# Kernel tuning notes

Measured on AMD Instinct MI355X. Metric: run time of the kernel, lower is better.

The kernel has to match this reference:

```python
import jax, jax.numpy as jnp
import numpy as np

T, B, IN = 64, 4096, 145
H1, H2 = 150, 32


def _lstm_layer(x, w_ih, w_hh, b_ih, b_hh):
    """Single LSTM layer, PyTorch gate order (i, f, g, o).
    x: (T, B, in_dim); w_ih: (4H, in_dim); w_hh: (4H, H); biases: (4H,).
    Returns hidden sequence (T, B, H)."""
    H = w_hh.shape[1]
    Bsz = x.shape[1]
    # Precompute input contribution for all timesteps at once (one big GEMM).
    xg = jnp.einsum('tbi,gi->tbg', x, w_ih) + (b_ih + b_hh)  # (T, B, 4H)
    w_hh_t = w_hh.T  # (H, 4H)

    def step(carry, xg_t):
        h, c = carry
        gates = xg_t + h @ w_hh_t  # (B, 4H)
        i, f, g, o = jnp.split(gates, 4, axis=-1)
        i = jax.nn.sigmoid(i)
        f = jax.nn.sigmoid(f)
        g = jnp.tanh(g)
        o = jax.nn.sigmoid(o)
        c = f * c + i * g
        h = o * jnp.tanh(c)
        return (h, c), h

    h0 = jnp.zeros((Bsz, H), x.dtype)
    c0 = jnp.zeros((Bsz, H), x.dtype)
    _, hs = jax.lax.scan(step, (h0, c0), xg)
    return hs  # (T, B, H)


def _init_lstm_params(key, in_dim, hidden):
    # PyTorch init: U(-k, k) with k = 1/sqrt(hidden)
    k = 1.0 / np.sqrt(hidden)
    ks = jax.random.split(key, 4)
    w_ih = jax.random.uniform(ks[0], (4 * hidden, in_dim), jnp.float32, -k, k)
    w_hh = jax.random.uniform(ks[1], (4 * hidden, hidden), jnp.float32, -k, k)
    b_ih = jax.random.uniform(ks[2], (4 * hidden,), jnp.float32, -k, k)
    b_hh = jax.random.uniform(ks[3], (4 * hidden,), jnp.float32, -k, k)
    return w_ih, w_hh, b_ih, b_hh


def setup_inputs() -> dict:
    key = jax.random.key(0)
    kx, k0, k1, k2 = jax.random.split(key, 4)
    x = jax.random.normal(kx, (T, B, IN), jnp.float32)
    w_ih_l0, w_hh_l0, b_ih_l0, b_hh_l0 = _init_lstm_params(k0, IN, H1)
    w_ih_l1, w_hh_l1, b_ih_l1, b_hh_l1 = _init_lstm_params(k1, H1, H1)
    w_ih_l2, w_hh_l2, b_ih_l2, b_hh_l2 = _init_lstm_params(k2, H1, H2)
    return {
        'x': x,
        'w_ih_l0': w_ih_l0, 'w_hh_l0': w_hh_l0, 'b_ih_l0': b_ih_l0, 'b_hh_l0': b_hh_l0,
        'w_ih_l1': w_ih_l1, 'w_hh_l1': w_hh_l1, 'b_ih_l1': b_ih_l1, 'b_hh_l1': b_hh_l1,
        'w_ih_l2': w_ih_l2, 'w_hh_l2': w_hh_l2, 'b_ih_l2': b_ih_l2, 'b_hh_l2': b_hh_l2,
    }


def reference(x,
              w_ih_l0, w_hh_l0, b_ih_l0, b_hh_l0,
              w_ih_l1, w_hh_l1, b_ih_l1, b_hh_l1,
              w_ih_l2, w_hh_l2, b_ih_l2, b_hh_l2):
    # temporal_model1: 2-layer LSTM (145 -> 150 -> 150)
    h = _lstm_layer(x, w_ih_l0, w_hh_l0, b_ih_l0, b_hh_l0)
    h = _lstm_layer(h, w_ih_l1, w_hh_l1, b_ih_l1, b_hh_l1)
    # temporal_model2: 1-layer LSTM (150 -> 32)
    out2 = _lstm_layer(h, w_ih_l2, w_hh_l2, b_ih_l2, b_hh_l2)
    return out2  # (T, B, 32)
```

## Files before the change

### kernel.cpp

```cpp
#include <hip/hip_runtime.h>


typedef _Float16 f16;
typedef _Float16 f16x8 __attribute__((ext_vector_type(8)));
typedef _Float16 f16x4 __attribute__((ext_vector_type(4)));
typedef float f32x4 __attribute__((ext_vector_type(4)));

#define T_STEPS 64
#define BATCH 4096

__device__ __forceinline__ float fexp(float x) {
  return __builtin_amdgcn_exp2f(x * 1.44269504088896340736f);
}
__device__ __forceinline__ float sigf(float x) {
  return __builtin_amdgcn_rcpf(1.0f + fexp(-x));
}
__device__ __forceinline__ float tanh_f(float x) {
  return 1.0f - 2.0f * __builtin_amdgcn_rcpf(1.0f + fexp(2.0f * x));
}

#define BAR_LGKM() asm volatile("s_waitcnt lgkmcnt(0)\n\ts_barrier" ::: "memory")

__global__ __launch_bounds__(256) void prep_w(
    const float* __restrict__ wih0, const float* __restrict__ bih0, const float* __restrict__ bhh0,
    const float* __restrict__ wih1, const float* __restrict__ bih1, const float* __restrict__ bhh1,
    f16* __restrict__ wprep0, f16* __restrict__ wprep1,
    float* __restrict__ bias0, float* __restrict__ bias1) {
  int idx = blockIdx.x * 256 + threadIdx.x;
  constexpr int WE = 640 * 168;
  if (idx < WE) {
    int c = idx / 168, k = idx - c * 168;
    int gate = c / 160, cg = c - gate * 160;
    float v = (cg < 150 && k < 145) ? wih0[(size_t)(gate * 150 + cg) * 145 + k] : 0.f;
    wprep0[idx] = (f16)v;
  } else if (idx < 2 * WE) {
    int e = idx - WE;
    int c = e / 168, k = e - c * 168;
    int gate = c / 160, cg = c - gate * 160;
    float v = (cg < 150 && k < 150) ? wih1[(size_t)(gate * 150 + cg) * 150 + k] : 0.f;
    wprep1[e] = (f16)v;
  } else if (idx < 2 * WE + 640) {
    int c = idx - 2 * WE;
    int gate = c / 160, cg = c - gate * 160;
    bias0[c] = (cg < 150) ? (bih0[gate * 150 + cg] + bhh0[gate * 150 + cg]) : 0.f;
  } else if (idx < 2 * WE + 1280) {
    int c = idx - 2 * WE - 640;
    int gate = c / 160, cg = c - gate * 160;
    bias1[c] = (cg < 150) ? (bih1[gate * 150 + cg] + bhh1[gate * 150 + cg]) : 0.f;
  }
}

template <int IN_DIM, int SRC_F16>
__global__ __launch_bounds__(512, 4) void gemm_xg4(
    const float* __restrict__ xin_f32, const f16* __restrict__ xin_f16,
    const f16* __restrict__ wprep, const float* __restrict__ bias_pre,
    f16* __restrict__ xg) {
  constexpr int ASTR = 168;
  __shared__ __align__(16) f16 A_lds[128 * ASTR];
  __shared__ __align__(16) f16 W_lds[64 * ASTR];
  __shared__ __align__(16) float bias_lds[640];
  const int tid = threadIdx.x;
  const int mtile = blockIdx.x;
  const int g0 = mtile * 128;

  if constexpr (SRC_F16) {
#pragma unroll
    for (int q = 0; q < 6; ++q) {
      int i = q * 512 + tid;
      if (i < 2688)
        *(f16x8*)(&A_lds[i * 8]) = *(const f16x8*)(xin_f16 + (size_t)g0 * ASTR + (size_t)i * 8);
    }
  } else {
#pragma unroll
    for (int q = 0; q < 10; ++q) {
      int idx = q * 512 + tid;
      int r = idx / 40, c4 = (idx - r * 40) * 4;
      f16x4 o;
      if (c4 + 4 <= IN_DIM) {
        f32x4 v;
        __builtin_memcpy(&v, xin_f32 + (size_t)(g0 + r) * IN_DIM + c4, 16);
#pragma unroll
        for (int j = 0; j < 4; ++j) o[j] = (f16)v[j];
      } else {
#pragma unroll
        for (int j = 0; j < 4; ++j)
          o[j] = (c4 + j < IN_DIM) ? (f16)xin_f32[(size_t)(g0 + r) * IN_DIM + c4 + j] : (f16)0.f;
      }
      *(f16x4*)(&A_lds[r * ASTR + c4]) = o;
    }
  }
  if (tid < 160) *(f32x4*)(&bias_lds[tid * 4]) = *(const f32x4*)(bias_pre + tid * 4);
#pragma unroll
  for (int q = 0; q < 3; ++q) {
    int i = q * 512 + tid;
    if (i < 1344) *(f16x8*)(&W_lds[i * 8]) = *(const f16x8*)(wprep + (size_t)i * 8);
  }
  BAR_LGKM();

  const int l = tid & 63, wv = tid >> 6;
  const int p = wv >> 1, cq = wv & 1;
  const int lrow = l & 15, lk8 = (l >> 4) * 8, r0 = (l >> 4) * 4;
  const int arow0 = (2 * p) * 16 + lrow;
  const int wrow0 = (2 * cq) * 16 + lrow;

  f16x8 pv0, pv1, pv2;
  for (int ch = 0; ch < 10; ++ch) {
    if (ch < 9) {
      const f16* wsrc = wprep + (size_t)(ch + 1) * 10752;
      pv0 = *(const f16x8*)(wsrc + (size_t)tid * 8);
      pv1 = *(const f16x8*)(wsrc + (size_t)(tid + 512) * 8);
      if (tid < 320) pv2 = *(const f16x8*)(wsrc + (size_t)(tid + 1024) * 8);
    }
    const int c0 = ch * 64 + (2 * cq) * 16 + lrow;
    const float bs0 = bias_lds[c0], bs1 = bias_lds[c0 + 16];
    f32x4 a00 = {bs0, bs0, bs0, bs0}, a01 = {bs1, bs1, bs1, bs1};
    f32x4 a10 = a00, a11 = a01;
#pragma unroll
    for (int kc = 0; kc < 5; ++kc) {
      f16x8 a0 = *(const f16x8*)(&A_lds[arow0 * ASTR + kc * 32 + lk8]);
      f16x8 a1 = *(const f16x8*)(&A_lds[(arow0 + 16) * ASTR + kc * 32 + lk8]);
      f16x8 b0 = *(const f16x8*)(&W_lds[wrow0 * ASTR + kc * 32 + lk8]);
      f16x8 b1 = *(const f16x8*)(&W_lds[(wrow0 + 16) * ASTR + kc * 32 + lk8]);
      a00 = __builtin_amdgcn_mfma_f32_16x16x32_f16(a0, b0, a00, 0, 0, 0);
      a01 = __builtin_amdgcn_mfma_f32_16x16x32_f16(a0, b1, a01, 0, 0, 0);
      a10 = __builtin_amdgcn_mfma_f32_16x16x32_f16(a1, b0, a10, 0, 0, 0);
      a11 = __builtin_amdgcn_mfma_f32_16x16x32_f16(a1, b1, a11, 0, 0, 0);
    }
    {
      f16x4 o;
      size_t rg0 = (size_t)(mtile * 8 + 2 * p);
#pragma unroll
      for (int j = 0; j < 4; ++j) o[j] = (f16)a00[j];
      *(f16x4*)(xg + (rg0 * 640 + c0) * 16 + r0) = o;
#pragma unroll
      for (int j = 0; j < 4; ++j) o[j] = (f16)a01[j];
      *(f16x4*)(xg + (rg0 * 640 + c0 + 16) * 16 + r0) = o;
#pragma unroll
      for (int j = 0; j < 4; ++j) o[j] = (f16)a10[j];
      *(f16x4*)(xg + ((rg0 + 1) * 640 + c0) * 16 + r0) = o;
#pragma unroll
      for (int j = 0; j < 4; ++j) o[j] = (f16)a11[j];
      *(f16x4*)(xg + ((rg0 + 1) * 640 + c0 + 16) * 16 + r0) = o;
    }
    if (ch < 9) {
      BAR_LGKM();
      *(f16x8*)(&W_lds[tid * 8]) = pv0;
      *(f16x8*)(&W_lds[(tid + 512) * 8]) = pv1;
      if (tid < 320) *(f16x8*)(&W_lds[(tid + 1024) * 8]) = pv2;
      BAR_LGKM();
    }
  }
}

__global__ __launch_bounds__(640, 2) void lstm_rec(
    const f16* __restrict__ xg, const float* __restrict__ whh,
    f16* __restrict__ hout) {
  constexpr int H = 150, HSTR = 168, CPAD = 640;
  __shared__ __align__(16) f16 hbuf[2][16 * HSTR];
  const int tid = threadIdx.x;
  const int l = tid & 63, w = tid >> 6;
  const int lrow = l & 15, lk8 = (l >> 4) * 8, r0 = (l >> 4) * 4;
  const int col = w * 16 + lrow;
  const int bx = blockIdx.x, b0 = bx * 16;

  for (int i = tid; i < 2 * 16 * HSTR / 8; i += 640) {
    f16x8 z = {};
    *(f16x8*)(&hbuf[0][0] + (size_t)i * 8) = z;
  }

  f16x8 wh[4][5];
#pragma unroll
  for (int g = 0; g < 4; ++g)
#pragma unroll
    for (int kc = 0; kc < 5; ++kc) {
      f16x8 v;
#pragma unroll
      for (int j = 0; j < 8; ++j) {
        int k = kc * 32 + lk8 + j;
        float x = (col < H && k < H) ? whh[((size_t)g * H + col) * H + k] : 0.f;
        v[j] = (f16)x;
      }
      wh[g][kc] = v;
    }
  __syncthreads();

  float creg[4] = {0.f, 0.f, 0.f, 0.f};
  f16x4 pv[4];
#pragma unroll
  for (int g = 0; g < 4; ++g)
    pv[g] = *(const f16x4*)(xg + ((size_t)bx * CPAD + g * 160 + col) * 16 + r0);

  for (int t = 0; t < T_STEPS; ++t) {
    const int cur = t & 1, nxt = cur ^ 1;

    f32x4 acc[4];
#pragma unroll
    for (int g = 0; g < 4; ++g) {
#pragma unroll
      for (int j = 0; j < 4; ++j) acc[g][j] = (float)pv[g][j];
    }
    if (t + 1 < T_STEPS) {
#pragma unroll
      for (int g = 0; g < 4; ++g)
        pv[g] = *(const f16x4*)(xg + ((size_t)((t + 1) * 256 + bx) * CPAD + g * 160 + col) * 16 + r0);
    }
    if (t > 0 && tid < 336) {
      f16x8 v = *(const f16x8*)(&hbuf[cur][tid * 8]);
      *(f16x8*)(hout + ((size_t)(t - 1) * BATCH + b0) * 168 + (size_t)tid * 8) = v;
    }

#pragma unroll
    for (int kc = 0; kc < 5; ++kc) {
      f16x8 a = *(const f16x8*)(&hbuf[cur][lrow * HSTR + kc * 32 + lk8]);
#pragma unroll
      for (int g = 0; g < 4; ++g)
        acc[g] = __builtin_amdgcn_mfma_f32_16x16x32_f16(a, wh[g][kc], acc[g], 0, 0, 0);
    }

#pragma unroll
    for (int j = 0; j < 4; ++j) {
      float iv = sigf(acc[0][j]);
      float fv = sigf(acc[1][j]);
      float gv = tanh_f(acc[2][j]);
      float ov = sigf(acc[3][j]);
      float c = fv * creg[j] + iv * gv;
      creg[j] = c;
      float h = ov * tanh_f(c);
      hbuf[nxt][(r0 + j) * HSTR + col] = (f16)h;
    }

    BAR_LGKM();
  }
  if (tid < 336) {
    f16x8 v = *(const f16x8*)(&hbuf[0][tid * 8]);
    *(f16x8*)(hout + ((size_t)(T_STEPS - 1) * BATCH + b0) * 168 + (size_t)tid * 8) = v;
  }
}

template <int IN_DIM, int H, int MODE>
__global__ __launch_bounds__(512, 2) void lstm_layer(
    const float* __restrict__ xin_f32, const f16* __restrict__ xin_f16,
    const float* __restrict__ w_ih, const float* __restrict__ w_hh,
    const float* __restrict__ b_ih, const float* __restrict__ b_hh,
    f16* __restrict__ hout, float* __restrict__ yout) {
  constexpr int KX = (IN_DIM + 31) / 32;
  constexpr int XSTR = KX * 32 + 8;
  constexpr int KH = (H + 31) / 32;
  constexpr int HSTR = KH * 32 + 8;
  constexpr int NPAD = ((H + 31) / 32) * 32;
  constexpr int NT = NPAD / 32;
  constexpr int GROUPS = NPAD * 4;
  constexpr int UPD_ITERS = (GROUPS + 511) / 512;
  constexpr int XIN_ELEMS = 16 * IN_DIM;
  constexpr int QX = (XIN_ELEMS + 511) / 512;
  constexpr int STG = (16 * XSTR) / 8;
  constexpr int HCP = (16 * HSTR) / 8;
  static_assert(MODE == 0 || XSTR == 168, "");

  __shared__ __align__(16) f16 xbuf[2][16 * XSTR];
  __shared__ __align__(16) f16 hbuf[16 * HSTR];
  __shared__ __align__(16) float gates[NPAD * 84];

  const int tid = threadIdx.x;
  const int l = tid & 63;
  const int wv = tid >> 6;
  const int gate = wv >> 1;
  const int half = wv & 1;
  const int lrow = l & 15;
  const int lk8 = (l >> 4) * 8;
  const int r0 = (l >> 4) * 4;
  const int b0 = blockIdx.x * 16;

  {
    f16* xf = &xbuf[0][0];
    for (int i = tid; i < 2 * 16 * XSTR; i += 512) xf[i] = (f16)0.f;
    for (int i = tid; i < 16 * HSTR; i += 512) hbuf[i] = (f16)0.f;
  }
  const int rbase = half * (NPAD / 2) + lrow;
  float bias_reg[NT];
#pragma unroll
  for (int nt = 0; nt < NT; ++nt) {
    int n = rbase + nt * 16;
    bias_reg[nt] = (n < H) ? (b_ih[gate * H + n] + b_hh[gate * H + n]) : 0.f;
  }
  f16x8 wx[KX][NT], wh[KH][NT];
#pragma unroll
  for (int kc = 0; kc < KX; ++kc)
#pragma unroll
    for (int nt = 0; nt < NT; ++nt) {
      f16x8 wq;
#pragma unroll
      for (int j = 0; j < 8; ++j) {
        int k = kc * 32 + lk8 + j;
        int r = rbase + nt * 16;
        float v = (r < H && k < IN_DIM) ? w_ih[(size_t)(gate * H + r) * IN_DIM + k] : 0.f;
        wq[j] = (f16)v;
      }
      wx[kc][nt] = wq;
    }
#pragma unroll
  for (int kc = 0; kc < KH; ++kc)
#pragma unroll
    for (int nt = 0; nt < NT; ++nt) {
      f16x8 wq;
#pragma unroll
      for (int j = 0; j < 8; ++j) {
        int k = kc * 32 + lk8 + j;
        int r = rbase + nt * 16;
        float v = (r < H && k < H) ? w_hh[(size_t)(gate * H + r) * H + k] : 0.f;
        wq[j] = (f16)v;
      }
      wh[kc][nt] = wq;
    }

  if constexpr (MODE == 0) {
#pragma unroll
    for (int q = 0; q < QX; ++q) {
      int idx = q * 512 + tid;
      if (idx < XIN_ELEMS) {
        float v = xin_f32[(size_t)b0 * IN_DIM + idx];
        int r = idx / IN_DIM, c = idx - r * IN_DIM;
        xbuf[0][r * XSTR + c] = (f16)v;
      }
    }
  } else {
    if (tid < STG) {
      f16x8 v = *(const f16x8*)(xin_f16 + (size_t)b0 * 168 + tid * 8);
      *(f16x8*)(&xbuf[0][tid * 8]) = v;
    }
  }
  __syncthreads();

  float creg[UPD_ITERS][4];
#pragma unroll
  for (int it = 0; it < UPD_ITERS; ++it)
#pragma unroll
    for (int j = 0; j < 4; ++j) creg[it][j] = 0.f;

  float xv[QX];
  f16x8 pv;

  for (int t = 0; t < T_STEPS; ++t) {
    const int cur = t & 1, nxt = cur ^ 1;
    if (t + 1 < T_STEPS) {
      if constexpr (MODE == 0) {
        const float* src = xin_f32 + ((size_t)(t + 1) * BATCH + b0) * IN_DIM;
#pragma unroll
        for (int q = 0; q < QX; ++q) {
          int idx = q * 512 + tid;
          xv[q] = (idx < XIN_ELEMS) ? src[idx] : 0.f;
        }
      } else {
        if (tid < STG)
          pv = *(const f16x8*)(xin_f16 + ((size_t)(t + 1) * BATCH + b0) * 168 + tid * 8);
      }
    }
    if constexpr (MODE != 2) {
      if (t > 0 && tid < HCP) {
        f16x8 v = *(const f16x8*)(&hbuf[tid * 8]);
        *(f16x8*)(hout + ((size_t)(t - 1) * BATCH + b0) * 168 + tid * 8) = v;
      }
    }
    f32x4 acc[NT];
#pragma unroll
    for (int nt = 0; nt < NT; ++nt) {
      float b = bias_reg[nt];
      acc[nt] = f32x4{b, b, b, b};
    }
    {
      const f16* xb = &xbuf[cur][0];
#pragma unroll
      for (int kc = 0; kc < KX; ++kc) {
        f16x8 a = *(const f16x8*)(xb + lrow * XSTR + kc * 32 + lk8);
#pragma unroll
        for (int nt = 0; nt < NT; ++nt)
          acc[nt] = __builtin_amdgcn_mfma_f32_16x16x32_f16(a, wx[kc][nt], acc[nt], 0, 0, 0);
      }
#pragma unroll
      for (int kc = 0; kc < KH; ++kc) {
        f16x8 a = *(const f16x8*)(hbuf + lrow * HSTR + kc * 32 + lk8);
#pragma unroll
        for (int nt = 0; nt < NT; ++nt)
          acc[nt] = __builtin_amdgcn_mfma_f32_16x16x32_f16(a, wh[kc][nt], acc[nt], 0, 0, 0);
      }
    }
#pragma unroll
    for (int nt = 0; nt < NT; ++nt) {
      int n = half * (NPAD / 2) + nt * 16 + lrow;
      *(f32x4*)(&gates[n * 84 + gate * 20 + r0]) = acc[nt];
    }
    BAR_LGKM();
    if (t + 1 < T_STEPS) {
      if constexpr (MODE == 0) {
#pragma unroll
        for (int q = 0; q < QX; ++q) {
          int idx = q * 512 + tid;
          if (idx < XIN_ELEMS) {
            int r = idx / IN_DIM, c = idx - r * IN_DIM;
            xbuf[nxt][r * XSTR + c] = (f16)xv[q];
          }
        }
      } else {
        if (tid < STG) *(f16x8*)(&xbuf[nxt][tid * 8]) = pv;
      }
    }
#pragma unroll
    for (int it = 0; it < UPD_ITERS; ++it) {
      int grp = it * 512 + tid;
      if (grp < GROUPS) {
        int n = grp % NPAD;
        int rb = (grp / NPAD) * 4;
        if (n < H) {
          f32x4 gi = *(const f32x4*)(&gates[n * 84 + 0 + rb]);
          f32x4 gf = *(const f32x4*)(&gates[n * 84 + 20 + rb]);
          f32x4 gg = *(const f32x4*)(&gates[n * 84 + 40 + rb]);
          f32x4 go = *(const f32x4*)(&gates[n * 84 + 60 + rb]);
#pragma unroll
          for (int j = 0; j < 4; ++j) {
            float iv = sigf(gi[j]);
            float fv = sigf(gf[j]);
            float gv = tanh_f(gg[j]);
            float ov = sigf(go[j]);
            float c = fv * creg[it][j] + iv * gv;
            creg[it][j] = c;
            float h = ov * tanh_f(c);
            hbuf[(rb + j) * HSTR + n] = (f16)h;
            if constexpr (MODE == 2) {
              yout[((size_t)t * BATCH + b0 + rb + j) * 32 + n] = h;
            }
          }
        }
      }
    }
    BAR_LGKM();
  }
  if constexpr (MODE != 2) {
    if (tid < HCP) {
      f16x8 v = *(const f16x8*)(&hbuf[tid * 8]);
      *(f16x8*)(hout + ((size_t)(T_STEPS - 1) * BATCH + b0) * 168 + tid * 8) = v;
    }
  }
}

extern "C" void kernel_launch(void* const* d_in, const int* in_sizes, int n_in,
                              void* d_out, int out_size, void* d_ws, size_t ws_size,
                              hipStream_t stream) {
  const float* x = (const float*)d_in[0];
  const float* wih0 = (const float*)d_in[1];
  const float* whh0 = (const float*)d_in[2];
  const float* bih0 = (const float*)d_in[3];
  const float* bhh0 = (const float*)d_in[4];
  const float* wih1 = (const float*)d_in[5];
  const float* whh1 = (const float*)d_in[6];
  const float* bih1 = (const float*)d_in[7];
  const float* bhh1 = (const float*)d_in[8];
  const float* wih2 = (const float*)d_in[9];
  const float* whh2 = (const float*)d_in[10];
  const float* bih2 = (const float*)d_in[11];
  const float* bhh2 = (const float*)d_in[12];

  const size_t HSEQ_BYTES = (size_t)T_STEPS * BATCH * 168 * sizeof(f16);
  const size_t XG_BYTES = (size_t)T_STEPS * BATCH * 640 * sizeof(f16);
  const size_t WPREP_BYTES = (size_t)640 * 168 * sizeof(f16);
  const size_t NEED = HSEQ_BYTES + XG_BYTES + 2 * WPREP_BYTES + 2 * 640 * sizeof(float);
  f16* hws = (f16*)d_ws;
  float* out = (float*)d_out;

  if (ws_size >= NEED) {
    char* base = (char*)d_ws;
    f16* xgbuf = (f16*)(base + HSEQ_BYTES);
    f16* wprep0 = (f16*)(base + HSEQ_BYTES + XG_BYTES);
    f16* wprep1 = (f16*)(base + HSEQ_BYTES + XG_BYTES + WPREP_BYTES);
    float* bias0 = (float*)(base + HSEQ_BYTES + XG_BYTES + 2 * WPREP_BYTES);
    float* bias1 = bias0 + 640;

    prep_w<<<dim3(846), dim3(256), 0, stream>>>(wih0, bih0, bhh0, wih1, bih1, bhh1,
                                                wprep0, wprep1, bias0, bias1);
    dim3 gg(2048), gb(512);
    dim3 rg(BATCH / 16), rb(640);
    gemm_xg4<145, 0><<<gg, gb, 0, stream>>>(x, nullptr, wprep0, bias0, xgbuf);
    lstm_rec<<<rg, rb, 0, stream>>>(xgbuf, whh0, hws);
    gemm_xg4<150, 1><<<gg, gb, 0, stream>>>(nullptr, hws, wprep1, bias1, xgbuf);
    lstm_rec<<<rg, rb, 0, stream>>>(xgbuf, whh1, hws);
    lstm_layer<150, 32, 2><<<dim3(BATCH / 16), dim3(512), 0, stream>>>(
        nullptr, hws, wih2, whh2, bih2, bhh2, nullptr, out);
  } else {
    dim3 grid(BATCH / 16), block(512);
    lstm_layer<145, 150, 0><<<grid, block, 0, stream>>>(x, nullptr, wih0, whh0, bih0, bhh0, hws, nullptr);
    lstm_layer<150, 150, 1><<<grid, block, 0, stream>>>(nullptr, hws, wih1, whh1, bih1, bhh1, hws, nullptr);
    lstm_layer<150, 32, 2><<<grid, block, 0, stream>>>(nullptr, hws, wih2, whh2, bih2, bhh2, nullptr, out);
  }
}
```

Before: 615.8 us.

## Fuse layer-2 input projection into layer-1 recurrence and add small layer-2 kernel

The layer-1 recurrent kernel now also computes the layer-2 input gates (150->128) with extra MFMAs from the freshly produced hidden state and writes them to a compact f16 buffer. The full h1 sequence write and reread are dropped. A new lightweight recurrence kernel for the 32-wide layer then uses 8 batch rows per block over twice as many blocks, where the old general lstm_layer kernel also did the input GEMM. This cuts memory traffic and the serial work in layer 2. The cost is extra MFMA and register pressure in the layer-1 recurrence, and half-idle lanes in the small kernel.

Result: no change. 613.7 us (-0.3%).

```diff
diff --git a/kernel.cpp b/kernel.cpp
--- a/kernel.cpp
+++ b/kernel.cpp
@@ -237,6 +237,207 @@
   }
 }
 
+__global__ __launch_bounds__(640, 2) void lstm_rec1f(
+    const f16* __restrict__ xg, const float* __restrict__ whh,
+    const float* __restrict__ wih2, const float* __restrict__ bih2,
+    const float* __restrict__ bhh2, f16* __restrict__ xg2) {
+  constexpr int H = 150, HSTR = 168, CPAD = 640;
+  __shared__ __align__(16) f16 hbuf[2][16 * HSTR];
+  const int tid = threadIdx.x;
+  const int l = tid & 63, w = tid >> 6;
+  const int lrow = l & 15, lk8 = (l >> 4) * 8, r0 = (l >> 4) * 4;
+  const int col = w * 16 + lrow;
+  const int bx = blockIdx.x;
+  const bool xw = (w < 8);
+  const int c2 = w * 16 + lrow;
+
+  for (int i = tid; i < 2 * 16 * HSTR / 8; i += 640) {
+    f16x8 z = {};
+    *(f16x8*)(&hbuf[0][0] + (size_t)i * 8) = z;
+  }
+
+  f16x8 wh[4][5];
+#pragma unroll
+  for (int g = 0; g < 4; ++g)
+#pragma unroll
+    for (int kc = 0; kc < 5; ++kc) {
+      f16x8 v;
+#pragma unroll
+      for (int j = 0; j < 8; ++j) {
+        int k = kc * 32 + lk8 + j;
+        float x = (col < H && k < H) ? whh[((size_t)g * H + col) * H + k] : 0.f;
+        v[j] = (f16)x;
+      }
+      wh[g][kc] = v;
+    }
+  f16x8 wx2[5];
+  float bias2 = 0.f;
+  if (xw) {
+#pragma unroll
+    for (int kc = 0; kc < 5; ++kc) {
+      f16x8 v;
+#pragma unroll
+      for (int j = 0; j < 8; ++j) {
+        int k = kc * 32 + lk8 + j;
+        float x = (k < 150) ? wih2[(size_t)c2 * 150 + k] : 0.f;
+        v[j] = (f16)x;
+      }
+      wx2[kc] = v;
+    }
+    bias2 = bih2[c2] + bhh2[c2];
+  }
+  __syncthreads();
+
+  float creg[4] = {0.f, 0.f, 0.f, 0.f};
+  f16x4 pv[4];
+#pragma unroll
+  for (int g = 0; g < 4; ++g)
+    pv[g] = *(const f16x4*)(xg + ((size_t)bx * CPAD + g * 160 + col) * 16 + r0);
+
+  for (int t = 0; t < T_STEPS; ++t) {
+    const int cur = t & 1, nxt = cur ^ 1;
+
+    f32x4 acc[4];
+#pragma unroll
+    for (int g = 0; g < 4; ++g) {
+#pragma unroll
+      for (int j = 0; j < 4; ++j) acc[g][j] = (float)pv[g][j];
+    }
+    if (t + 1 < T_STEPS) {
+#pragma unroll
+      for (int g = 0; g < 4; ++g)
+        pv[g] = *(const f16x4*)(xg + ((size_t)((t + 1) * 256 + bx) * CPAD + g * 160 + col) * 16 + r0);
+    }
+
+    f32x4 accx = {bias2, bias2, bias2, bias2};
+#pragma unroll
+    for (int kc = 0; kc < 5; ++kc) {
+      f16x8 a = *(const f16x8*)(&hbuf[cur][lrow * HSTR + kc * 32 + lk8]);
+#pragma unroll
+      for (int g = 0; g < 4; ++g)
+        acc[g] = __builtin_amdgcn_mfma_f32_16x16x32_f16(a, wh[g][kc], acc[g], 0, 0, 0);
+      if (xw)
+        accx = __builtin_amdgcn_mfma_f32_16x16x32_f16(a, wx2[kc], accx, 0, 0, 0);
+    }
+    if (xw && t > 0) {
+      f16x4 o;
+#pragma unroll
+      for (int j = 0; j < 4; ++j) o[j] = (f16)accx[j];
+      *(f16x4*)(xg2 + (((size_t)(t - 1) * 256 + bx) * 128 + c2) * 16 + r0) = o;
+    }
+
+#pragma unroll
+    for (int j = 0; j < 4; ++j) {
+      float iv = sigf(acc[0][j]);
+      float fv = sigf(acc[1][j]);
+      float gv = tanh_f(acc[2][j]);
+      float ov = sigf(acc[3][j]);
+      float c = fv * creg[j] + iv * gv;
+      creg[j] = c;
+      float h = ov * tanh_f(c);
+      hbuf[nxt][(r0 + j) * HSTR + col] = (f16)h;
+    }
+
+    BAR_LGKM();
+  }
+  if (xw) {
+    f32x4 accx = {bias2, bias2, bias2, bias2};
+#pragma unroll
+    for (int kc = 0; kc < 5; ++kc) {
+      f16x8 a = *(const f16x8*)(&hbuf[0][lrow * HSTR + kc * 32 + lk8]);
+      accx = __builtin_amdgcn_mfma_f32_16x16x32_f16(a, wx2[kc], accx, 0, 0, 0);
+    }
+    f16x4 o;
+#pragma unroll
+    for (int j = 0; j < 4; ++j) o[j] = (f16)accx[j];
+    *(f16x4*)(xg2 + (((size_t)(T_STEPS - 1) * 256 + bx) * 128 + c2) * 16 + r0) = o;
+  }
+}
+
+__global__ __launch_bounds__(128) void lstm_rec32(
+    const f16* __restrict__ xg2, const float* __restrict__ whh2,
+    float* __restrict__ yout) {
+  constexpr int HSTR2 = 40;
+  __shared__ __align__(16) f16 hbuf2[2][16 * HSTR2];
+  const int tid = threadIdx.x;
+  const int l = tid & 63, w = tid >> 6;
+  const int lrow = l & 15, lk8 = (l >> 4) * 8, r0 = (l >> 4) * 4;
+  const int cg = w * 16 + lrow;
+  const int p = blockIdx.x;
+  const int rg = p >> 1, half = p & 1;
+  const int b0 = p * 8;
+  const bool active = (l < 32);
+
+  for (int i = tid; i < 2 * 16 * HSTR2 / 8; i += 128) {
+    f16x8 z = {};
+    *(f16x8*)(&hbuf2[0][0] + (size_t)i * 8) = z;
+  }
+
+  f16x8 wh2[4];
+#pragma unroll
+  for (int g = 0; g < 4; ++g) {
+    f16x8 v;
+#pragma unroll
+    for (int j = 0; j < 8; ++j)
+      v[j] = (f16)whh2[(size_t)(g * 32 + cg) * 32 + lk8 + j];
+    wh2[g] = v;
+  }
+  __syncthreads();
+
+  float creg[4] = {0.f, 0.f, 0.f, 0.f};
+  f16x4 pv[4];
+  if (active) {
+#pragma unroll
+    for (int g = 0; g < 4; ++g)
+      pv[g] = *(const f16x4*)(xg2 + ((size_t)rg * 128 + g * 32 + cg) * 16 + half * 8 + r0);
+  }
+
+  for (int t = 0; t < T_STEPS; ++t) {
+    const int cur = t & 1, nxt = cur ^ 1;
+
+    f32x4 acc[4];
+    if (active) {
+#pragma unroll
+      for (int g = 0; g < 4; ++g) {
+#pragma unroll
+        for (int j = 0; j < 4; ++j) acc[g][j] = (float)pv[g][j];
+      }
+      if (t + 1 < T_STEPS) {
+#pragma unroll
+        for (int g = 0; g < 4; ++g)
+          pv[g] = *(const f16x4*)(xg2 + (((size_t)(t + 1) * 256 + rg) * 128 + g * 32 + cg) * 16 + half * 8 + r0);
+      }
+    } else {
+#pragma unroll
+      for (int g = 0; g < 4; ++g) acc[g] = f32x4{0.f, 0.f, 0.f, 0.f};
+    }
+
+    {
+      f16x8 a = *(const f16x8*)(&hbuf2[cur][lrow * HSTR2 + lk8]);
+#pragma unroll
+      for (int g = 0; g < 4; ++g)
+        acc[g] = __builtin_amdgcn_mfma_f32_16x16x32_f16(a, wh2[g], acc[g], 0, 0, 0);
+    }
+
+    if (active) {
+#pragma unroll
+      for (int j = 0; j < 4; ++j) {
+        float iv = sigf(acc[0][j]);
+        float fv = sigf(acc[1][j]);
+        float gv = tanh_f(acc[2][j]);
+        float ov = sigf(acc[3][j]);
+        float c = fv * creg[j] + iv * gv;
+        creg[j] = c;
+        float h = ov * tanh_f(c);
+        hbuf2[nxt][(r0 + j) * HSTR2 + cg] = (f16)h;
+        yout[((size_t)t * BATCH + b0 + r0 + j) * 32 + cg] = h;
+      }
+    }
+
+    BAR_LGKM();
+  }
+}
+
 template <int IN_DIM, int H, int MODE>
 __global__ __launch_bounds__(512, 2) void lstm_layer(
     const float* __restrict__ xin_f32, const f16* __restrict__ xin_f16,
@@ -473,6 +674,7 @@
     f16* wprep1 = (f16*)(base + HSEQ_BYTES + XG_BYTES + WPREP_BYTES);
     float* bias0 = (float*)(base + HSEQ_BYTES + XG_BYTES + 2 * WPREP_BYTES);
     float* bias1 = bias0 + 640;
+    f16* xg2buf = hws;
 
     prep_w<<<dim3(846), dim3(256), 0, stream>>>(wih0, bih0, bhh0, wih1, bih1, bhh1,
                                                 wprep0, wprep1, bias0, bias1);
@@ -481,9 +683,8 @@
     gemm_xg4<145, 0><<<gg, gb, 0, stream>>>(x, nullptr, wprep0, bias0, xgbuf);
     lstm_rec<<<rg, rb, 0, stream>>>(xgbuf, whh0, hws);
     gemm_xg4<150, 1><<<gg, gb, 0, stream>>>(nullptr, hws, wprep1, bias1, xgbuf);
-    lstm_rec<<<rg, rb, 0, stream>>>(xgbuf, whh1, hws);
-    lstm_layer<150, 32, 2><<<dim3(BATCH / 16), dim3(512), 0, stream>>>(
-        nullptr, hws, wih2, whh2, bih2, bhh2, nullptr, out);
+    lstm_rec1f<<<rg, rb, 0, stream>>>(xgbuf, whh1, wih2, bih2, bhh2, xg2buf);
+    lstm_rec32<<<dim3(BATCH / 8), dim3(128), 0, stream>>>(xg2buf, whh2, out);
   } else {
     dim3 grid(BATCH / 16), block(512);
     lstm_layer<145, 150, 0><<<grid, block, 0, stream>>>(x, nullptr, wih0, whh0, bih0, bhh0, hws, nullptr);
```
